# Performance work log

Hardware: AMD Instinct MI355X
Metric: run time of the kernel (lower is better)

The kernel has to match this reference:

```python
import jax, jax.numpy as jnp
import numpy as np

DIM = 192
HEADS = 4
EPS = 1e-12  # F.normalize default eps


def setup_inputs() -> dict:
    key = jax.random.key(0)
    k0, k1, k2, k3 = jax.random.split(key, 4)
    x = jax.random.normal(k0, (4, DIM, 128, 128), dtype=jnp.float32)
    # qkv 1x1 conv weight: [3*dim, dim, 1, 1] -> stored as [3*dim, dim]
    w_qkv = jax.random.normal(k1, (3 * DIM, DIM), dtype=jnp.float32) * (1.0 / np.sqrt(DIM))
    # depthwise 3x3 conv weight: [3*dim, 1, 3, 3]
    w_dw = jax.random.normal(k2, (3 * DIM, 1, 3, 3), dtype=jnp.float32) * (1.0 / 3.0)
    # project_out 1x1 conv weight: [dim, dim]
    w_proj = jax.random.normal(k3, (DIM, DIM), dtype=jnp.float32) * (1.0 / np.sqrt(DIM))
    # temperature: ones(heads,1,1), requires_grad=False in original
    temperature = jnp.ones((HEADS, 1, 1), dtype=jnp.float32)
    return {"x": x, "w_qkv": w_qkv, "w_dw": w_dw, "w_proj": w_proj,
            "temperature": temperature}


def _l2norm(t):
    # F.normalize(t, dim=-1): t / max(||t||_2, eps)
    n = jnp.sqrt(jnp.sum(t * t, axis=-1, keepdims=True))
    return t / jnp.maximum(n, EPS)


def reference(x, w_qkv, w_dw, w_proj, temperature):
    b, c, h, w = x.shape
    ch = c // HEADS  # channels per head
    # 1x1 conv (no bias) == channel GEMM
    qkv = jnp.einsum('oc,bchw->bohw', w_qkv, x)
    # depthwise 3x3 conv, padding=1, groups=3*dim
    qkv = jax.lax.conv_general_dilated(
        qkv, w_dw, window_strides=(1, 1), padding=((1, 1), (1, 1)),
        dimension_numbers=('NCHW', 'OIHW', 'NCHW'),
        feature_group_count=3 * c)
    q, k, v = jnp.split(qkv, 3, axis=1)
    # b (head ch) h w -> b head ch (h w)
    def rearr(t):
        return t.reshape(b, HEADS, ch, h * w)
    q, k, v = rearr(q), rearr(k), rearr(v)
    q = _l2norm(q)
    k = _l2norm(k)
    # channel-channel attention: [b, head, ch, ch]
    attn = jnp.einsum('bhcn,bhdn->bhcd', q, k) * temperature[None]
    attn = jax.nn.softmax(attn, axis=-1)
    out = jnp.einsum('bhcd,bhdn->bhcn', attn, v)
    out = out.reshape(b, c, h, w)
    out = jnp.einsum('oc,bchw->bohw', w_proj, out)
    return out
```

## Files before the change

kernel.cpp:

```cpp
#include <hip/hip_runtime.h>

typedef unsigned short u16;
typedef float f32x4 __attribute__((ext_vector_type(4)));
typedef __bf16 bf16x8 __attribute__((ext_vector_type(8)));
typedef unsigned short u16x8 __attribute__((ext_vector_type(8)));
typedef unsigned short u16x4 __attribute__((ext_vector_type(4)));

#define DEV static __device__ __forceinline__

DEV u16 f2bf(float f) {
  unsigned int u = __float_as_uint(f);
  u += 0x7FFFu + ((u >> 16) & 1u);
  return (u16)(u >> 16);
}
DEV float bf2f(u16 h) { return __uint_as_float(((unsigned int)h) << 16); }

DEV void gload_lds16(const void* g, void* l) {
  __builtin_amdgcn_global_load_lds(
      (__attribute__((address_space(1))) void*)(unsigned long long)g,
      (__attribute__((address_space(3))) void*)l, 16, 0, 0);
}

__global__ __launch_bounds__(256) void convert_w_kernel(
    const float* __restrict__ in, u16* __restrict__ out, int n) {
  int i = blockIdx.x * 256 + threadIdx.x;
  if (i < n) out[i] = f2bf(in[i]);
}

__global__ __launch_bounds__(256) void transpose_f32_kernel(
    const float* __restrict__ in, u16* __restrict__ out,
    size_t inBatch, size_t outBatch, int C) {
  __shared__ u16 ls[64][66];
  const int b = blockIdx.z;
  const int c0 = blockIdx.x * 64, r0 = blockIdx.y * 64;
  const float* ip = in + (size_t)b * inBatch;
  u16* op = out + (size_t)b * outBatch;
  const int t = threadIdx.x;
  const int rr = t >> 4, cg = t & 15;
#pragma unroll
  for (int i = 0; i < 4; ++i) {
    const int r = i * 16 + rr;
    const f32x4 v = *(const f32x4*)(ip + (size_t)(r0 + r) * C + c0 + cg * 4);
    ls[r][cg * 4 + 0] = f2bf(v.x);
    ls[r][cg * 4 + 1] = f2bf(v.y);
    ls[r][cg * 4 + 2] = f2bf(v.z);
    ls[r][cg * 4 + 3] = f2bf(v.w);
  }
  __syncthreads();
  const int lane = t & 63, w = t >> 6;
#pragma unroll
  for (int i = 0; i < 16; ++i) {
    const int c = i * 4 + w;
    op[(size_t)(c0 + c) * 192 + r0 + lane] = ls[lane][c];
  }
}

__global__ __launch_bounds__(256) void transpose_u16_kernel(
    const u16* __restrict__ in, u16* __restrict__ out,
    size_t inBatch, size_t outBatch, int C) {
  __shared__ u16 ls[64][66];
  const int b = blockIdx.z;
  const int c0 = blockIdx.x * 64, r0 = blockIdx.y * 64;
  const u16* ip = in + (size_t)b * inBatch;
  u16* op = out + (size_t)b * outBatch;
  const int t = threadIdx.x;
  const int rr = t >> 3, cg = t & 7;
#pragma unroll
  for (int i = 0; i < 2; ++i) {
    const int r = i * 32 + rr;
    const u16x8 v = *(const u16x8*)(ip + (size_t)(r0 + r) * C + c0 + cg * 8);
#pragma unroll
    for (int j = 0; j < 8; ++j) ls[r][cg * 8 + j] = v[j];
  }
  __syncthreads();
  const int lane = t & 63, w = t >> 6;
#pragma unroll
  for (int i = 0; i < 16; ++i) {
    const int c = i * 4 + w;
    op[(size_t)(c0 + c) * 192 + r0 + lane] = ls[lane][c];
  }
}

template <bool OUT_BF16, int NJ>
__global__ __launch_bounds__(256, 2) void gemm_bt_kernel(
    const u16* __restrict__ A, const u16* __restrict__ B, void* __restrict__ Cv,
    size_t aBatch, size_t bBatch, size_t cBatch, int ldC) {
  __shared__ __align__(16) char smem[73728];
  char* sA = smem;
  char* sB = smem + 49152;

  const int tid = threadIdx.x, wave = tid >> 6, lane = tid & 63;
  const int id = blockIdx.x;
  const int m0 = (id & 127) * 128, b = id >> 7;
  const char* Ab = (const char*)(A + (size_t)b * aBatch + (size_t)m0 * 192);
  const char* Bbase = (const char*)(B + (size_t)b * bBatch);

#pragma unroll
  for (int i = 0; i < 12; ++i) {
    const int c = i * 4 + wave;
    const int d = c * 1024 + lane * 16;
    const int row = d / 384, inrow = d - row * 384;
    gload_lds16(Ab + row * 384 + (inrow ^ ((row & 7) << 4)), sA + c * 1024);
  }
#pragma unroll
  for (int i = 0; i < 6; ++i) {
    const int c = i * 4 + wave;
    const int d = c * 1024 + lane * 16;
    const int row = d / 384, inrow = d - row * 384;
    gload_lds16(Bbase + row * 384 + (inrow ^ ((row & 7) << 4)), sB + c * 1024);
  }
  asm volatile("s_waitcnt vmcnt(0)" ::: "memory");
  __builtin_amdgcn_s_barrier();

  const int wm = wave & 1, wn = wave >> 1;
  const int l15 = lane & 15, lg = lane >> 4;
  const int swm = (l15 & 7) << 4;
  const int rA0 = (wm * 64 + l15) * 384;
  const int rB0 = (wn * 32 + l15) * 384;

  bf16x8 af[4][6];
#pragma unroll
  for (int mi = 0; mi < 4; ++mi)
#pragma unroll
    for (int ks = 0; ks < 6; ++ks)
      af[mi][ks] = *(const bf16x8*)(sA + rA0 + mi * 16 * 384 +
                                    ((ks * 64 + lg * 16) ^ swm));

  f32x4 acc[4][2];
  for (int j = 0; j < NJ; ++j) {
    if (j > 0) {
      const int j0 = (j - 1) * 64;
      if (OUT_BF16) {
        u16* Cb = (u16*)Cv + (size_t)b * cBatch;
#pragma unroll
        for (int mi = 0; mi < 4; ++mi)
#pragma unroll
          for (int nj = 0; nj < 2; ++nj) {
            u16x4 ov;
#pragma unroll
            for (int r = 0; r < 4; ++r) ov[r] = f2bf(acc[mi][nj][r]);
            *(u16x4*)(Cb + (size_t)(j0 + wn * 32 + nj * 16 + l15) * ldC + m0 +
                      wm * 64 + mi * 16 + lg * 4) = ov;
          }
      } else {
        float* Cb = (float*)Cv + (size_t)b * cBatch;
#pragma unroll
        for (int mi = 0; mi < 4; ++mi)
#pragma unroll
          for (int nj = 0; nj < 2; ++nj)
            *(f32x4*)(Cb + (size_t)(j0 + wn * 32 + nj * 16 + l15) * ldC + m0 +
                      wm * 64 + mi * 16 + lg * 4) = acc[mi][nj];
      }
    }
    bf16x8 bfv[2][6];
#pragma unroll
    for (int nj = 0; nj < 2; ++nj)
#pragma unroll
      for (int ks = 0; ks < 6; ++ks)
        bfv[nj][ks] = *(const bf16x8*)(sB + rB0 + nj * 16 * 384 +
                                       ((ks * 64 + lg * 16) ^ swm));
    asm volatile("s_waitcnt lgkmcnt(0)" ::: "memory");
    __builtin_amdgcn_s_barrier();
    if (j + 1 < NJ) {
      const char* Bj = Bbase + (size_t)(j + 1) * 64 * 384;
#pragma unroll
      for (int i = 0; i < 6; ++i) {
        const int c = i * 4 + wave;
        const int d = c * 1024 + lane * 16;
        const int row = d / 384, inrow = d - row * 384;
        gload_lds16(Bj + row * 384 + (inrow ^ ((row & 7) << 4)), sB + c * 1024);
      }
    }
    __builtin_amdgcn_sched_barrier(0);
#pragma unroll
    for (int mi = 0; mi < 4; ++mi)
#pragma unroll
      for (int nj = 0; nj < 2; ++nj) acc[mi][nj] = (f32x4){0.f, 0.f, 0.f, 0.f};
#pragma unroll
    for (int ks = 0; ks < 6; ++ks)
#pragma unroll
      for (int mi = 0; mi < 4; ++mi)
#pragma unroll
        for (int nj = 0; nj < 2; ++nj)
          acc[mi][nj] = __builtin_amdgcn_mfma_f32_16x16x32_bf16(
              af[mi][ks], bfv[nj][ks], acc[mi][nj], 0, 0, 0);
    if (j + 1 < NJ) {
      asm volatile("s_waitcnt vmcnt(0)" ::: "memory");
      __builtin_amdgcn_s_barrier();
    }
  }
  {
    const int j0 = (NJ - 1) * 64;
    if (OUT_BF16) {
      u16* Cb = (u16*)Cv + (size_t)b * cBatch;
#pragma unroll
      for (int mi = 0; mi < 4; ++mi)
#pragma unroll
        for (int nj = 0; nj < 2; ++nj) {
          u16x4 ov;
#pragma unroll
          for (int r = 0; r < 4; ++r) ov[r] = f2bf(acc[mi][nj][r]);
          *(u16x4*)(Cb + (size_t)(j0 + wn * 32 + nj * 16 + l15) * ldC + m0 +
                    wm * 64 + mi * 16 + lg * 4) = ov;
        }
    } else {
      float* Cb = (float*)Cv + (size_t)b * cBatch;
#pragma unroll
      for (int mi = 0; mi < 4; ++mi)
#pragma unroll
        for (int nj = 0; nj < 2; ++nj)
          *(f32x4*)(Cb + (size_t)(j0 + wn * 32 + nj * 16 + l15) * ldC + m0 +
                    wm * 64 + mi * 16 + lg * 4) = acc[mi][nj];
    }
  }
}

__global__ __launch_bounds__(256) void dwconv_kernel(
    u16* __restrict__ qkv, const float* __restrict__ wdw,
    float* __restrict__ sq) {
  __shared__ u16 img[16384];
  __shared__ float red[4];
  const int o = blockIdx.x, b = blockIdx.y;
  const size_t base = ((size_t)b * 576 + o) * 16384;
  const int tid = threadIdx.x, wave = tid >> 6, lane = tid & 63;
#pragma unroll
  for (int i = 0; i < 8; ++i) {
    const int off = (i * 4 + wave) * 1024;
    gload_lds16((const char*)qkv + base * 2 + off + lane * 16, (char*)img + off);
  }
  asm volatile("s_waitcnt vmcnt(0)" ::: "memory");
  __syncthreads();
  float w[9];
#pragma unroll
  for (int j = 0; j < 9; ++j) w[j] = wdw[o * 9 + j];
  float sqacc = 0.f;
  for (int it = 0; it < 8; ++it) {
    const int chunk = it * 256 + tid;
    const int px0 = chunk * 8;
    const int y = px0 >> 7, x0 = px0 & 127;
    float acc[8];
#pragma unroll
    for (int j = 0; j < 8; ++j) acc[j] = 0.f;
#pragma unroll
    for (int dy = -1; dy <= 1; ++dy) {
      const int yy = y + dy;
      float v[10];
      if (yy >= 0 && yy <= 127) {
        const u16* rowp = img + yy * 128 + x0;
        u16x8 m = *(const u16x8*)rowp;
#pragma unroll
        for (int j = 0; j < 8; ++j) v[j + 1] = bf2f(m[j]);
        v[0] = (x0 > 0) ? bf2f(rowp[-1]) : 0.f;
        v[9] = (x0 < 120) ? bf2f(rowp[8]) : 0.f;
      } else {
#pragma unroll
        for (int j = 0; j < 10; ++j) v[j] = 0.f;
      }
      const float w0 = w[(dy + 1) * 3], w1 = w[(dy + 1) * 3 + 1],
                  w2 = w[(dy + 1) * 3 + 2];
#pragma unroll
      for (int j = 0; j < 8; ++j) acc[j] += w0 * v[j] + w1 * v[j + 1] + w2 * v[j + 2];
    }
    u16x8 ov;
#pragma unroll
    for (int j = 0; j < 8; ++j) {
      sqacc += acc[j] * acc[j];
      ov[j] = f2bf(acc[j]);
    }
    *(u16x8*)(qkv + base + px0) = ov;
  }
#pragma unroll
  for (int s = 32; s > 0; s >>= 1) sqacc += __shfl_xor(sqacc, s, 64);
  if (lane == 0) red[wave] = sqacc;
  __syncthreads();
  if (tid == 0) sq[b * 576 + o] = red[0] + red[1] + red[2] + red[3];
}

__global__ __launch_bounds__(256) void gram_kernel(
    const u16* __restrict__ qkv, float* __restrict__ partial) {
  __shared__ u16 tiles[4 * 3072];
  __shared__ float red[4 * 2304];
  const int bh = blockIdx.y, b = bh >> 2, h = bh & 3;
  const int g = blockIdx.x;
  const int wave = threadIdx.x >> 6, lane = threadIdx.x & 63;
  const int n0 = g * 1024 + wave * 256;
  const u16* qb = qkv + ((size_t)b * 576 + h * 48) * 16384;
  const u16* kb = qb + (size_t)192 * 16384;
  char* tl = (char*)(tiles + wave * 3072);
  const int l15 = lane & 15, lg = lane >> 4;
  const int swz = (l15 & 3) << 4;
  f32x4 acc[3][3];
#pragma unroll
  for (int i = 0; i < 3; ++i)
#pragma unroll
    for (int j = 0; j < 3; ++j) acc[i][j] = (f32x4){0.f, 0.f, 0.f, 0.f};

  for (int ks = 0; ks < 8; ++ks) {
    const int nn = n0 + ks * 32;
    asm volatile("s_waitcnt lgkmcnt(0)" ::: "memory");
#pragma unroll
    for (int i = 0; i < 6; ++i) {
      const int flat = i * 1024 + lane * 16;
      const int row = flat >> 6, colb = flat & 63;
      const u16* src = (row < 48) ? (qb + (size_t)row * 16384 + nn)
                                  : (kb + (size_t)(row - 48) * 16384 + nn);
      gload_lds16((const char*)src + (colb ^ ((row & 3) << 4)), tl + i * 1024);
    }
    asm volatile("s_waitcnt vmcnt(0)" ::: "memory");
    bf16x8 qf[3], kf[3];
#pragma unroll
    for (int f = 0; f < 3; ++f) {
      qf[f] = *(const bf16x8*)(tl + (f * 16 + l15) * 64 + ((lg * 16) ^ swz));
      kf[f] = *(const bf16x8*)(tl + (48 + f * 16 + l15) * 64 + ((lg * 16) ^ swz));
    }
#pragma unroll
    for (int i = 0; i < 3; ++i)
#pragma unroll
      for (int j = 0; j < 3; ++j)
        acc[i][j] = __builtin_amdgcn_mfma_f32_16x16x32_bf16(qf[i], kf[j],
                                                            acc[i][j], 0, 0, 0);
  }
  {
    float* rw = red + wave * 2304;
#pragma unroll
    for (int i = 0; i < 3; ++i)
#pragma unroll
      for (int j = 0; j < 3; ++j)
#pragma unroll
        for (int r = 0; r < 4; ++r)
          rw[(i * 16 + lg * 4 + r) * 48 + (j * 16 + l15)] = acc[i][j][r];
  }
  __syncthreads();
#pragma unroll
  for (int it = 0; it < 9; ++it) {
    const int p = it * 256 + threadIdx.x;
    const float s = red[p] + red[2304 + p] + red[4608 + p] + red[6912 + p];
    partial[((size_t)bh * 2304 + p) * 16 + g] = s;
  }
}

__global__ __launch_bounds__(256) void softmax_weff_kernel(
    const float* __restrict__ partial, const float* __restrict__ sq,
    const float* __restrict__ temp, const float* __restrict__ wproj,
    u16* __restrict__ weff) {
  __shared__ float G[2304];
  __shared__ float wp[192 * 49];
  __shared__ float nq[48], nk[48];
  const int bh = blockIdx.x, b = bh >> 2, h = bh & 3;
  const int tid = threadIdx.x;
#pragma unroll
  for (int it = 0; it < 36; ++it) {
    const int j = it * 256 + tid;
    const int o = j / 48, c = j - o * 48;
    wp[o * 49 + c] = wproj[o * 192 + h * 48 + c];
  }
#pragma unroll
  for (int it = 0; it < 9; ++it) {
    const int p = it * 256 + tid;
    const f32x4* pp = (const f32x4*)(partial + ((size_t)bh * 2304 + p) * 16);
    const f32x4 a = pp[0] + pp[1] + pp[2] + pp[3];
    G[p] = a.x + a.y + a.z + a.w;
  }
  if (tid < 48) {
    nq[tid] = fmaxf(sqrtf(sq[b * 576 + h * 48 + tid]), 1e-12f);
    nk[tid] = fmaxf(sqrtf(sq[b * 576 + 192 + h * 48 + tid]), 1e-12f);
  }
  __syncthreads();
  if (tid < 48) {
    const int r = tid;
    const float inq = temp[h] / nq[r];
    float L[48];
    float mx = -3.4e38f;
#pragma unroll 4
    for (int d = 0; d < 48; ++d) {
      const float v = G[r * 48 + d] * inq / nk[d];
      L[d] = v;
      mx = fmaxf(mx, v);
    }
    float s = 0.f;
#pragma unroll 4
    for (int d = 0; d < 48; ++d) {
      const float e = __expf(L[d] - mx);
      L[d] = e;
      s += e;
    }
    const float inv = 1.f / s;
#pragma unroll 4
    for (int d = 0; d < 48; ++d) G[r * 48 + d] = L[d] * inv;
  }
  __syncthreads();
  if (tid < 192) {
    const int o = tid;
    f32x4 acc[12];
#pragma unroll
    for (int dv = 0; dv < 12; ++dv) acc[dv] = (f32x4){0.f, 0.f, 0.f, 0.f};
    for (int c = 0; c < 48; ++c) {
      const float w = wp[o * 49 + c];
      const f32x4* at = (const f32x4*)(G + c * 48);
#pragma unroll
      for (int dv = 0; dv < 12; ++dv) acc[dv] += w * at[dv];
    }
    u16* op = weff + ((size_t)b * 192 + o) * 192 + h * 48;
#pragma unroll
    for (int g8 = 0; g8 < 6; ++g8) {
      u16x8 ov;
#pragma unroll
      for (int j = 0; j < 8; ++j) {
        const int d = g8 * 8 + j;
        ov[j] = f2bf(acc[d >> 2][d & 3]);
      }
      *(u16x8*)(op + g8 * 8) = ov;
    }
  }
}

extern "C" void kernel_launch(void* const* d_in, const int* in_sizes, int n_in,
                              void* d_out, int out_size, void* d_ws,
                              size_t ws_size, hipStream_t stream) {
  (void)in_sizes; (void)n_in; (void)out_size; (void)ws_size;
  const float* x      = (const float*)d_in[0];
  const float* w_qkv  = (const float*)d_in[1];
  const float* w_dw   = (const float*)d_in[2];
  const float* w_proj = (const float*)d_in[3];
  const float* temp   = (const float*)d_in[4];

  char* ws = (char*)d_ws;
  u16*   qkv     = (u16*)ws;
  u16*   vT      = (u16*)(ws + 75497472);
  float* partial = (float*)(ws + 100663296);
  float* sq      = (float*)(ws + 103022592);
  u16*   Wq      = (u16*)(ws + 103031808);
  u16*   Weff    = (u16*)(ws + 103252992);
  u16*   Xt      = (u16*)d_out;

  convert_w_kernel<<<dim3(432), 256, 0, stream>>>(w_qkv, Wq, 110592);
  transpose_f32_kernel<<<dim3(256, 3, 4), 256, 0, stream>>>(
      x, Xt, (size_t)192 * 16384, (size_t)16384 * 192, 16384);
  gemm_bt_kernel<true, 9><<<dim3(512), 256, 0, stream>>>(
      Xt, Wq, qkv, (size_t)16384 * 192, 0, (size_t)576 * 16384, 16384);
  dwconv_kernel<<<dim3(576, 4), 256, 0, stream>>>(qkv, w_dw, sq);
  gram_kernel<<<dim3(16, 16), 256, 0, stream>>>(qkv, partial);
  softmax_weff_kernel<<<dim3(16), 256, 0, stream>>>(partial, sq, temp, w_proj,
                                                    Weff);
  transpose_u16_kernel<<<dim3(256, 3, 4), 256, 0, stream>>>(
      qkv + (size_t)384 * 16384, vT, (size_t)576 * 16384, (size_t)16384 * 192,
      16384);
  gemm_bt_kernel<false, 3><<<dim3(512), 256, 0, stream>>>(
      vT, Weff, d_out, (size_t)16384 * 192, (size_t)192 * 192,
      (size_t)192 * 16384, 16384);
}
```

Measured before the change: 138.8 us.

## Fuse input transposes into GEMM loads and double gram kernel split

Drops the two standalone transpose kernels. The GEMM now reads channel-major fp32 x (or bf16 v) directly, converts and transposes in registers, and writes into the swizzled LDS tile. This removes two full-tensor round trips through global memory and two launches, at the cost of strided global reads and scalar LDS stores in place of async global-to-LDS copies. The gram kernel also uses 32 spatial chunks instead of 16, giving more blocks with shorter loops, and the softmax kernel sums the larger partial buffer.

```diff
diff --git a/kernel.cpp b/kernel.cpp
--- a/kernel.cpp
+++ b/kernel.cpp
@@ -27,64 +27,11 @@
   if (i < n) out[i] = f2bf(in[i]);
 }
 
-__global__ __launch_bounds__(256) void transpose_f32_kernel(
-    const float* __restrict__ in, u16* __restrict__ out,
-    size_t inBatch, size_t outBatch, int C) {
-  __shared__ u16 ls[64][66];
-  const int b = blockIdx.z;
-  const int c0 = blockIdx.x * 64, r0 = blockIdx.y * 64;
-  const float* ip = in + (size_t)b * inBatch;
-  u16* op = out + (size_t)b * outBatch;
-  const int t = threadIdx.x;
-  const int rr = t >> 4, cg = t & 15;
-#pragma unroll
-  for (int i = 0; i < 4; ++i) {
-    const int r = i * 16 + rr;
-    const f32x4 v = *(const f32x4*)(ip + (size_t)(r0 + r) * C + c0 + cg * 4);
-    ls[r][cg * 4 + 0] = f2bf(v.x);
-    ls[r][cg * 4 + 1] = f2bf(v.y);
-    ls[r][cg * 4 + 2] = f2bf(v.z);
-    ls[r][cg * 4 + 3] = f2bf(v.w);
-  }
-  __syncthreads();
-  const int lane = t & 63, w = t >> 6;
-#pragma unroll
-  for (int i = 0; i < 16; ++i) {
-    const int c = i * 4 + w;
-    op[(size_t)(c0 + c) * 192 + r0 + lane] = ls[lane][c];
-  }
-}
-
-__global__ __launch_bounds__(256) void transpose_u16_kernel(
-    const u16* __restrict__ in, u16* __restrict__ out,
-    size_t inBatch, size_t outBatch, int C) {
-  __shared__ u16 ls[64][66];
-  const int b = blockIdx.z;
-  const int c0 = blockIdx.x * 64, r0 = blockIdx.y * 64;
-  const u16* ip = in + (size_t)b * inBatch;
-  u16* op = out + (size_t)b * outBatch;
-  const int t = threadIdx.x;
-  const int rr = t >> 3, cg = t & 7;
-#pragma unroll
-  for (int i = 0; i < 2; ++i) {
-    const int r = i * 32 + rr;
-    const u16x8 v = *(const u16x8*)(ip + (size_t)(r0 + r) * C + c0 + cg * 8);
-#pragma unroll
-    for (int j = 0; j < 8; ++j) ls[r][cg * 8 + j] = v[j];
-  }
-  __syncthreads();
-  const int lane = t & 63, w = t >> 6;
-#pragma unroll
-  for (int i = 0; i < 16; ++i) {
-    const int c = i * 4 + w;
-    op[(size_t)(c0 + c) * 192 + r0 + lane] = ls[lane][c];
-  }
-}
-
-template <bool OUT_BF16, int NJ>
+template <bool IN_F32, bool OUT_BF16, int NJ>
 __global__ __launch_bounds__(256, 2) void gemm_bt_kernel(
-    const u16* __restrict__ A, const u16* __restrict__ B, void* __restrict__ Cv,
-    size_t aBatch, size_t bBatch, size_t cBatch, int ldC) {
+    const void* __restrict__ Av, const u16* __restrict__ B,
+    void* __restrict__ Cv, size_t aBatch, size_t bBatch, size_t cBatch,
+    int ldC) {
   __shared__ __align__(16) char smem[73728];
   char* sA = smem;
   char* sB = smem + 49152;
@@ -92,16 +39,51 @@
   const int tid = threadIdx.x, wave = tid >> 6, lane = tid & 63;
   const int id = blockIdx.x;
   const int m0 = (id & 127) * 128, b = id >> 7;
-  const char* Ab = (const char*)(A + (size_t)b * aBatch + (size_t)m0 * 192);
+
+  if (IN_F32) {
+    const float* Xb = (const float*)Av + (size_t)b * aBatch + m0;
+    const int cbl = tid & 7, iq = tid >> 3;
+#pragma unroll
+    for (int pass = 0; pass < 6; ++pass) {
+      const int cb = pass * 8 + cbl;
+      f32x4 v[4];
+#pragma unroll
+      for (int r = 0; r < 4; ++r)
+        v[r] = *(const f32x4*)(Xb + (size_t)(cb * 4 + r) * 16384 + iq * 4);
+#pragma unroll
+      for (int j = 0; j < 4; ++j) {
+        const int n = iq * 4 + j;
+        u16x4 col;
+        col[0] = f2bf(v[0][j]);
+        col[1] = f2bf(v[1][j]);
+        col[2] = f2bf(v[2][j]);
+        col[3] = f2bf(v[3][j]);
+        *(u16x4*)(sA + n * 384 + ((cb * 8) ^ ((n & 7) << 4))) = col;
+      }
+    }
+  } else {
+    const u16* Vb = (const u16*)Av + (size_t)b * aBatch + m0;
+    const int cbl = tid & 15, iq = tid >> 4;
+#pragma unroll
+    for (int pass = 0; pass < 3; ++pass) {
+      const int cb = pass * 16 + cbl;
+      u16x8 v[4];
+#pragma unroll
+      for (int r = 0; r < 4; ++r)
+        v[r] = *(const u16x8*)(Vb + (size_t)(cb * 4 + r) * 16384 + iq * 8);
+#pragma unroll
+      for (int j = 0; j < 8; ++j) {
+        const int n = iq * 8 + j;
+        u16x4 col;
+        col[0] = v[0][j];
+        col[1] = v[1][j];
+        col[2] = v[2][j];
+        col[3] = v[3][j];
+        *(u16x4*)(sA + n * 384 + ((cb * 8) ^ ((n & 7) << 4))) = col;
+      }
+    }
+  }
   const char* Bbase = (const char*)(B + (size_t)b * bBatch);
-
-#pragma unroll
-  for (int i = 0; i < 12; ++i) {
-    const int c = i * 4 + wave;
-    const int d = c * 1024 + lane * 16;
-    const int row = d / 384, inrow = d - row * 384;
-    gload_lds16(Ab + row * 384 + (inrow ^ ((row & 7) << 4)), sA + c * 1024);
-  }
 #pragma unroll
   for (int i = 0; i < 6; ++i) {
     const int c = i * 4 + wave;
@@ -109,7 +91,7 @@
     const int row = d / 384, inrow = d - row * 384;
     gload_lds16(Bbase + row * 384 + (inrow ^ ((row & 7) << 4)), sB + c * 1024);
   }
-  asm volatile("s_waitcnt vmcnt(0)" ::: "memory");
+  asm volatile("s_waitcnt vmcnt(0) lgkmcnt(0)" ::: "memory");
   __builtin_amdgcn_s_barrier();
 
   const int wm = wave & 1, wn = wave >> 1;
@@ -283,7 +265,7 @@
   const int bh = blockIdx.y, b = bh >> 2, h = bh & 3;
   const int g = blockIdx.x;
   const int wave = threadIdx.x >> 6, lane = threadIdx.x & 63;
-  const int n0 = g * 1024 + wave * 256;
+  const int n0 = g * 512 + wave * 128;
   const u16* qb = qkv + ((size_t)b * 576 + h * 48) * 16384;
   const u16* kb = qb + (size_t)192 * 16384;
   char* tl = (char*)(tiles + wave * 3072);
@@ -295,7 +277,7 @@
 #pragma unroll
     for (int j = 0; j < 3; ++j) acc[i][j] = (f32x4){0.f, 0.f, 0.f, 0.f};
 
-  for (int ks = 0; ks < 8; ++ks) {
+  for (int ks = 0; ks < 4; ++ks) {
     const int nn = n0 + ks * 32;
     asm volatile("s_waitcnt lgkmcnt(0)" ::: "memory");
 #pragma unroll
@@ -335,7 +317,7 @@
   for (int it = 0; it < 9; ++it) {
     const int p = it * 256 + threadIdx.x;
     const float s = red[p] + red[2304 + p] + red[4608 + p] + red[6912 + p];
-    partial[((size_t)bh * 2304 + p) * 16 + g] = s;
+    partial[((size_t)bh * 2304 + p) * 32 + g] = s;
   }
 }
 
@@ -357,8 +339,9 @@
 #pragma unroll
   for (int it = 0; it < 9; ++it) {
     const int p = it * 256 + tid;
-    const f32x4* pp = (const f32x4*)(partial + ((size_t)bh * 2304 + p) * 16);
-    const f32x4 a = pp[0] + pp[1] + pp[2] + pp[3];
+    const f32x4* pp = (const f32x4*)(partial + ((size_t)bh * 2304 + p) * 32);
+    const f32x4 a = (pp[0] + pp[1]) + (pp[2] + pp[3]) +
+                    (pp[4] + pp[5]) + (pp[6] + pp[7]);
     G[p] = a.x + a.y + a.z + a.w;
   }
   if (tid < 48) {
@@ -426,26 +409,19 @@
 
   char* ws = (char*)d_ws;
   u16*   qkv     = (u16*)ws;
-  u16*   vT      = (u16*)(ws + 75497472);
-  float* partial = (float*)(ws + 100663296);
-  float* sq      = (float*)(ws + 103022592);
-  u16*   Wq      = (u16*)(ws + 103031808);
-  u16*   Weff    = (u16*)(ws + 103252992);
-  u16*   Xt      = (u16*)d_out;
+  float* partial = (float*)(ws + 75497472);
+  float* sq      = (float*)(ws + 80216064);
+  u16*   Wq      = (u16*)(ws + 80225280);
+  u16*   Weff    = (u16*)(ws + 80446464);
 
   convert_w_kernel<<<dim3(432), 256, 0, stream>>>(w_qkv, Wq, 110592);
-  transpose_f32_kernel<<<dim3(256, 3, 4), 256, 0, stream>>>(
-      x, Xt, (size_t)192 * 16384, (size_t)16384 * 192, 16384);
-  gemm_bt_kernel<true, 9><<<dim3(512), 256, 0, stream>>>(
-      Xt, Wq, qkv, (size_t)16384 * 192, 0, (size_t)576 * 16384, 16384);
+  gemm_bt_kernel<true, true, 9><<<dim3(512), 256, 0, stream>>>(
+      x, Wq, qkv, (size_t)192 * 16384, 0, (size_t)576 * 16384, 16384);
   dwconv_kernel<<<dim3(576, 4), 256, 0, stream>>>(qkv, w_dw, sq);
-  gram_kernel<<<dim3(16, 16), 256, 0, stream>>>(qkv, partial);
+  gram_kernel<<<dim3(32, 16), 256, 0, stream>>>(qkv, partial);
   softmax_weff_kernel<<<dim3(16), 256, 0, stream>>>(partial, sq, temp, w_proj,
                                                     Weff);
-  transpose_u16_kernel<<<dim3(256, 3, 4), 256, 0, stream>>>(
-      qkv + (size_t)384 * 16384, vT, (size_t)576 * 16384, (size_t)16384 * 192,
-      16384);
-  gemm_bt_kernel<false, 3><<<dim3(512), 256, 0, stream>>>(
-      vT, Weff, d_out, (size_t)16384 * 192, (size_t)192 * 192,
-      (size_t)192 * 16384, 16384);
-}
+  gemm_bt_kernel<false, false, 3><<<dim3(512), 256, 0, stream>>>(
+      qkv + (size_t)384 * 16384, Weff, d_out, (size_t)576 * 16384,
+      (size_t)192 * 192, (size_t)192 * 16384, 16384);
+}
```

Result: no change. 137.3 us (-1.1%).
